# Optimization experiments

Measured on AMD Instinct MI355X. Metric: run time of the kernel, lower is better.

The kernel has to match this reference:

```python
import jax, jax.numpy as jnp
import numpy as np

B, N, DIM = 4, 2048, 768
H, C = 12, 64            # num_heads, head_dim
M = 384                  # num random features = dim * kernel_ratio
SCALE = C ** (-0.25)
EPS = 1e-8
INV_SQRT_M = 1.0 / np.sqrt(M).astype(np.float32)


def _make_orf(key):
    # per-head orthogonal random features: rows of each (C, M) block are
    # orthonormal (C <= M), scaled by sqrt(M), matching sample_orf's intent.
    g = jax.random.normal(key, (H, M, C), jnp.float32)
    q = jnp.linalg.qr(g)[0]                 # (H, M, C), orthonormal columns
    return jnp.transpose(q, (0, 2, 1)) * np.float32(np.sqrt(M))  # (H, C, M)


def setup_inputs() -> dict:
    key = jax.random.key(0)
    k0, k1, k2, k3 = jax.random.split(key, 4)
    x = jax.random.normal(k0, (B, N, DIM), jnp.float32)
    w = _make_orf(k1)                                       # (H, C, M), frozen
    Wqkv = jax.random.normal(k2, (DIM, 3 * DIM), jnp.float32) * 0.02
    Wproj = jax.random.normal(k3, (DIM, DIM), jnp.float32) * 0.02
    bproj = jnp.zeros((DIM,), jnp.float32)
    return {"x": x, "w": w, "Wqkv": Wqkv, "Wproj": Wproj, "bproj": bproj}


def _kernel(x, w):
    # x: (B, H, N, C) -> phi(x): (B, H, N, M)
    xs = x * SCALE
    proj = jnp.einsum('bhnc,hcm->bhnm', xs, w)
    sq_half = 0.5 * jnp.sum(xs * xs, axis=-1, keepdims=True)  # (B,H,N,1)
    return jnp.exp(proj - sq_half) * INV_SQRT_M


def reference(x, w, Wqkv, Wproj, bproj):
    qkv = (x @ Wqkv).reshape(B, N, 3, H, C).transpose(2, 0, 3, 1, 4)
    q, k, v = qkv[0], qkv[1], qkv[2]
    qf = _kernel(q, w)                       # (B, H, N, M)
    kf = _kernel(k, w)                       # (B, H, N, M)
    # normalizer D_n = q'_n . sum_j k'_j
    D = jnp.einsum('bhnm,bhm->bhn', qf, jnp.sum(kf, axis=2)) + EPS
    # linear attention: (k'^T v) then q' @ (k'^T v)
    ktv = jnp.einsum('bhnm,bhnc->bhmc', kf, v)      # (B, H, M, C)
    out = jnp.einsum('bhnm,bhmc->bhnc', qf, ktv) / D[..., None]
    out = out.transpose(0, 2, 1, 3).reshape(B, N, DIM)
    return out @ Wproj + bproj
```

## Files before the change

### kernel.cpp

```cpp
#include <hip/hip_runtime.h>

typedef __attribute__((ext_vector_type(8))) short s16x8;
typedef __attribute__((ext_vector_type(4))) float f32x4;

#define MFMA(a, b, c) __builtin_amdgcn_mfma_f32_16x16x32_bf16(a, b, c, 0, 0, 0)

namespace {

constexpr int Bn = 4, Nn = 2048, Hn = 12, Mn = 384;
constexpr float SCALE = 0.35355339059327379f;
constexpr float ISM = 0.05103103630798288f;
constexpr float EPS = 1e-8f;

__device__ inline unsigned short f2b(float f) {
  unsigned u = __builtin_bit_cast(unsigned, f);
  return (unsigned short)((u + 0x7fffu + ((u >> 16) & 1u)) >> 16);
}
__device__ inline float b2f(unsigned short h) {
  unsigned u = ((unsigned)h) << 16;
  return __builtin_bit_cast(float, u);
}

__device__ inline void gl_lds16(const unsigned short* g, unsigned short* l) {
  __builtin_amdgcn_global_load_lds(
      (const __attribute__((address_space(1))) unsigned int*)g,
      (__attribute__((address_space(3))) unsigned int*)l, 16, 0, 0);
}

__global__ __launch_bounds__(256) void cvt_all_k(const float* __restrict__ x,
                                                 const float* __restrict__ Wqkv,
                                                 const float* __restrict__ Wproj,
                                                 const float* __restrict__ w,
                                                 unsigned short* __restrict__ xb,
                                                 unsigned short* __restrict__ wqT,
                                                 unsigned short* __restrict__ wpT,
                                                 unsigned short* __restrict__ wt) {
  const int bid = blockIdx.x;
  if (bid < 3072) {
    const int id = bid * 256 + threadIdx.x;
    const float* src = x + (size_t)id * 8;
    s16x8 o;
#pragma unroll
    for (int j = 0; j < 8; ++j) o[j] = (short)f2b(src[j]);
    *(s16x8*)(xb + (size_t)id * 8) = o;
  } else if (bid < 3936) {
    const int id = (bid - 3072) * 256 + threadIdx.x;
    const int n = id / 96, kc = (id % 96) * 8;
    s16x8 o;
#pragma unroll
    for (int j = 0; j < 8; ++j) o[j] = (short)f2b(Wqkv[(size_t)(kc + j) * 2304 + n]);
    *(s16x8*)(wqT + (size_t)n * 768 + kc) = o;
  } else if (bid < 4224) {
    const int id = (bid - 3936) * 256 + threadIdx.x;
    const int n = id / 96, kc = (id % 96) * 8;
    s16x8 o;
#pragma unroll
    for (int j = 0; j < 8; ++j) o[j] = (short)f2b(Wproj[(size_t)(kc + j) * 768 + n]);
    *(s16x8*)(wpT + (size_t)n * 768 + kc) = o;
  } else {
    const int id = (bid - 4224) * 256 + threadIdx.x;
    const int h = id / (384 * 8);
    const int r = id % (384 * 8);
    const int m = r / 8, cc = (r % 8) * 8;
    s16x8 o;
#pragma unroll
    for (int j = 0; j < 8; ++j) o[j] = (short)f2b(w[((size_t)h * 64 + cc + j) * 384 + m]);
    *(s16x8*)(wt + ((size_t)h * 384 + m) * 64 + cc) = o;
  }
}

__global__ __launch_bounds__(256) void gemm_qkv_k(const unsigned short* __restrict__ A,
                                                  const unsigned short* __restrict__ Bt,
                                                  unsigned short* __restrict__ obf) {
  __shared__ unsigned short ldsA[128 * 64];
  __shared__ unsigned short ldsB[128 * 64];
  char* lA = (char*)ldsA;
  char* lB = (char*)ldsB;
  const int t = threadIdx.x, lane = t & 63, w = t >> 6;
  const int ln = lane & 15, kg = lane >> 4;
  const int flat = blockIdx.y * 18 + blockIdx.x;
  const int swz = (flat & 7) * 144 + (flat >> 3);
  const size_t bm = (size_t)(swz / 18) * 128, bn = (size_t)(swz % 18) * 128;
  const int wr = w >> 1, wc = w & 1;
  const int sr = lane >> 3, s = lane & 7;
  f32x4 acc[4][4];
#pragma unroll
  for (int i = 0; i < 4; ++i)
#pragma unroll
    for (int j = 0; j < 4; ++j) acc[i][j] = (f32x4){0.f, 0.f, 0.f, 0.f};

  for (int kb = 0; kb < 768; kb += 64) {
    __syncthreads();
#pragma unroll
    for (int c = 0; c < 4; ++c) {
      const int row = c * 32 + w * 8 + sr;
      const int ss = (s ^ (row & 7)) * 8;
      gl_lds16(A + (bm + row) * 768 + kb + ss, ldsA + (c * 4 + w) * 512);
      gl_lds16(Bt + (bn + row) * 768 + kb + ss, ldsB + (c * 4 + w) * 512);
    }
    __syncthreads();
#pragma unroll
    for (int ks = 0; ks < 2; ++ks) {
      s16x8 af[4], bfr[4];
#pragma unroll
      for (int mi = 0; mi < 4; ++mi) {
        const int row = wr * 64 + mi * 16 + ln;
        af[mi] = *(const s16x8*)(lA + row * 128 + (((ks * 4 + kg) ^ (row & 7)) << 4));
      }
#pragma unroll
      for (int ni = 0; ni < 4; ++ni) {
        const int row = wc * 64 + ni * 16 + ln;
        bfr[ni] = *(const s16x8*)(lB + row * 128 + (((ks * 4 + kg) ^ (row & 7)) << 4));
      }
#pragma unroll
      for (int mi = 0; mi < 4; ++mi)
#pragma unroll
        for (int ni = 0; ni < 4; ++ni) acc[mi][ni] = MFMA(af[mi], bfr[ni], acc[mi][ni]);
    }
  }
#pragma unroll
  for (int mi = 0; mi < 4; ++mi)
#pragma unroll
    for (int ni = 0; ni < 4; ++ni) {
      const size_t orow0 = bm + wr * 64 + mi * 16 + kg * 4;
      const size_t ocol = bn + wc * 64 + ni * 16 + ln;
#pragma unroll
      for (int r = 0; r < 4; ++r) obf[(orow0 + r) * 2304 + ocol] = f2b(acc[mi][ni][r]);
    }
}

__global__ __launch_bounds__(256) void gemm_proj_k(const unsigned short* __restrict__ A,
                                                   const unsigned short* __restrict__ Bt,
                                                   float* __restrict__ out,
                                                   const float* __restrict__ bias) {
  __shared__ unsigned short ldsA[128 * 64];
  __shared__ unsigned short ldsB[64 * 64];
  char* lA = (char*)ldsA;
  char* lB = (char*)ldsB;
  const int t = threadIdx.x, lane = t & 63, w = t >> 6;
  const int ln = lane & 15, kg = lane >> 4;
  const int flat = blockIdx.y * 12 + blockIdx.x;
  const int swz = (flat & 7) * 96 + (flat >> 3);
  const size_t bm = (size_t)(swz / 12) * 128, bn = (size_t)(swz % 12) * 64;
  const int wr = w >> 1, wc = w & 1;
  const int sr = lane >> 3, s = lane & 7;
  f32x4 acc[4][2];
#pragma unroll
  for (int i = 0; i < 4; ++i)
#pragma unroll
    for (int j = 0; j < 2; ++j) acc[i][j] = (f32x4){0.f, 0.f, 0.f, 0.f};

  for (int kb = 0; kb < 768; kb += 64) {
    __syncthreads();
#pragma unroll
    for (int c = 0; c < 4; ++c) {
      const int row = c * 32 + w * 8 + sr;
      const int ss = (s ^ (row & 7)) * 8;
      gl_lds16(A + (bm + row) * 768 + kb + ss, ldsA + (c * 4 + w) * 512);
    }
#pragma unroll
    for (int c = 0; c < 2; ++c) {
      const int row = c * 32 + w * 8 + sr;
      const int ss = (s ^ (row & 7)) * 8;
      gl_lds16(Bt + (bn + row) * 768 + kb + ss, ldsB + (c * 4 + w) * 512);
    }
    __syncthreads();
#pragma unroll
    for (int ks = 0; ks < 2; ++ks) {
      s16x8 af[4], bfr[2];
#pragma unroll
      for (int mi = 0; mi < 4; ++mi) {
        const int row = wr * 64 + mi * 16 + ln;
        af[mi] = *(const s16x8*)(lA + row * 128 + (((ks * 4 + kg) ^ (row & 7)) << 4));
      }
#pragma unroll
      for (int ni = 0; ni < 2; ++ni) {
        const int row = wc * 32 + ni * 16 + ln;
        bfr[ni] = *(const s16x8*)(lB + row * 128 + (((ks * 4 + kg) ^ (row & 7)) << 4));
      }
#pragma unroll
      for (int mi = 0; mi < 4; ++mi)
#pragma unroll
        for (int ni = 0; ni < 2; ++ni) acc[mi][ni] = MFMA(af[mi], bfr[ni], acc[mi][ni]);
    }
  }
#pragma unroll
  for (int mi = 0; mi < 4; ++mi)
#pragma unroll
    for (int ni = 0; ni < 2; ++ni) {
      const size_t orow0 = bm + wr * 64 + mi * 16 + kg * 4;
      const size_t ocol = bn + wc * 32 + ni * 16 + ln;
      const float bv = bias[ocol];
#pragma unroll
      for (int r = 0; r < 4; ++r) out[(orow0 + r) * 768 + ocol] = acc[mi][ni][r] + bv;
    }
}

template <int NCT, int CT0>
__device__ inline void s2_gemm2(const char* kfT_b, const char* vt_b, int mts, int ln, int kg,
                                f32x4 (*acc)[3]) {
#pragma unroll
  for (int half = 0; half < 2; ++half) {
    s16x8 a[3], bb[NCT];
#pragma unroll
    for (int j = 0; j < 3; ++j) {
      const int m = (mts + j) * 16 + ln;
      a[j] = *(const s16x8*)(kfT_b + m * 128 + ((half * 64 + kg * 16) ^ ((m & 7) << 4)));
    }
#pragma unroll
    for (int i = 0; i < NCT; ++i) {
      const int c = (CT0 + i) * 16 + ln;
      bb[i] = *(const s16x8*)(vt_b + c * 128 + ((half * 64 + kg * 16) ^ ((c & 7) << 4)));
    }
#pragma unroll
    for (int j = 0; j < 3; ++j)
#pragma unroll
      for (int i = 0; i < NCT; ++i) acc[j][i] = MFMA(a[j], bb[i], acc[j][i]);
  }
}

__global__ __launch_bounds__(512, 4) void stage2_k(const unsigned short* __restrict__ qkv,
                                                   const unsigned short* __restrict__ wt,
                                                   float* __restrict__ ktv_part,
                                                   float* __restrict__ ksum_part) {
  __shared__ unsigned short kfT[192 * 64];
  __shared__ unsigned short vt[80 * 64];
  __shared__ unsigned short wt_s[192 * 64];
  __shared__ unsigned short k_s[64 * 64];
  __shared__ float sqh[64];
  char* kfT_b = (char*)kfT;
  char* vt_b = (char*)vt;
  char* wt_b = (char*)wt_s;
  char* k_b = (char*)k_s;
  const int t = threadIdx.x, lane = t & 63, w = t >> 6;
  const int ln = lane & 15, kg = lane >> 4;
  const int gx = blockIdx.x, h = blockIdx.y, b = blockIdx.z;
  const int ng = gx >> 1, mh = gx & 1, m0 = mh * 192;
  const int bh = b * Hn + h;
  const int ntile = w & 3, mgrp = w >> 2;
  const int mts = (w & 3) * 3;
  const int cg = w >> 2;
  const int lr = lane >> 3, sl = lane & 7;

  auto stage_k = [&](int ch) {
    const int row = w * 8 + lr;
    gl_lds16(qkv + ((size_t)b * Nn + ng * 512 + ch * 64 + row) * 2304 + 768 + h * 64 +
                 ((sl ^ (row & 7)) * 8),
             k_s + w * 512);
  };
  const int vn = t >> 3, vc0 = (t & 7) * 8;
  auto load_v = [&](int ch) {
    return *(const s16x8*)(qkv + ((size_t)b * Nn + ng * 512 + ch * 64 + vn) * 2304 + 1536 +
                           h * 64 + vc0);
  };
  auto scat_v = [&](s16x8 vv) {
#pragma unroll
    for (int j = 0; j < 8; ++j) {
      const int c = vc0 + j;
      *(unsigned short*)(vt_b + c * 128 + ((2 * vn) ^ ((c & 7) << 4))) = (unsigned short)vv[j];
    }
  };
  auto do_sq = [&]() {
    const int n = t >> 3, slq = t & 7;
    const s16x8 kk = *(const s16x8*)(k_b + n * 128 + ((slq ^ (n & 7)) << 4));
    float sacc = 0.f;
#pragma unroll
    for (int j = 0; j < 8; ++j) {
      const float f = b2f((unsigned short)kk[j]);
      sacc = fmaf(f, f, sacc);
    }
    sacc += __shfl_xor(sacc, 1);
    sacc += __shfl_xor(sacc, 2);
    sacc += __shfl_xor(sacc, 4);
    if ((t & 7) == 0) sqh[n] = 0.5f * SCALE * SCALE * sacc;
  };

#pragma unroll
  for (int rr = 0; rr < 3; ++rr) {
    const int j = w * 3 + rr;
    const int row = j * 8 + lr;
    gl_lds16(wt + ((size_t)h * 384 + m0 + row) * 64 + ((sl ^ (row & 7)) * 8), wt_s + j * 512);
  }
  for (int i = t; i < 1024; i += 512) {
    const int c = 64 + (i >> 6), nn = i & 63;
    *(unsigned short*)(vt_b + c * 128 + ((2 * nn) ^ ((c & 7) << 4))) =
        (c == 64) ? (unsigned short)0x3F80 : (unsigned short)0;
  }
  stage_k(0);
  s16x8 vreg = load_v(0);
  __syncthreads();
  scat_v(vreg);
  do_sq();
  __syncthreads();

  f32x4 acc[3][3];
#pragma unroll
  for (int j = 0; j < 3; ++j)
#pragma unroll
    for (int i = 0; i < 3; ++i) acc[j][i] = (f32x4){0.f, 0.f, 0.f, 0.f};

  for (int ch = 0; ch < 8; ++ch) {
    {
      const int arow = ntile * 16 + ln;
      const s16x8 a0 = *(const s16x8*)(k_b + arow * 128 + ((kg ^ (arow & 7)) << 4));
      const s16x8 a1 = *(const s16x8*)(k_b + arow * 128 + (((kg + 4) ^ (arow & 7)) << 4));
      const int nr = ntile * 16 + kg * 4;
      const float s0 = sqh[nr], s1 = sqh[nr + 1], s2 = sqh[nr + 2], s3 = sqh[nr + 3];
#pragma unroll
      for (int i = 0; i < 6; ++i) {
        const int mloc = (mgrp * 6 + i) * 16 + ln;
        const s16x8 b0 = *(const s16x8*)(wt_b + mloc * 128 + ((kg ^ (mloc & 7)) << 4));
        const s16x8 b1 = *(const s16x8*)(wt_b + mloc * 128 + (((kg + 4) ^ (mloc & 7)) << 4));
        f32x4 p = (f32x4){0.f, 0.f, 0.f, 0.f};
        p = MFMA(a0, b0, p);
        p = MFMA(a1, b1, p);
        const float e0 = __expf(fmaf(SCALE, p[0], -s0)) * ISM;
        const float e1 = __expf(fmaf(SCALE, p[1], -s1)) * ISM;
        const float e2 = __expf(fmaf(SCALE, p[2], -s2)) * ISM;
        const float e3 = __expf(fmaf(SCALE, p[3], -s3)) * ISM;
        uint2 pk;
        pk.x = (unsigned)f2b(e0) | ((unsigned)f2b(e1) << 16);
        pk.y = (unsigned)f2b(e2) | ((unsigned)f2b(e3) << 16);
        const int bytn = 32 * ntile + 8 * kg;
        *(uint2*)(kfT_b + mloc * 128 + (bytn ^ ((mloc & 7) << 4))) = pk;
      }
    }
    __syncthreads();
    if (ch < 7) {
      stage_k(ch + 1);
      vreg = load_v(ch + 1);
    }
    if (cg == 0)
      s2_gemm2<3, 0>(kfT_b, vt_b, mts, ln, kg, acc);
    else
      s2_gemm2<2, 3>(kfT_b, vt_b, mts, ln, kg, acc);
    __syncthreads();
    if (ch < 7) {
      scat_v(vreg);
      do_sq();
      __syncthreads();
    }
  }
  float* base = ktv_part + ((size_t)ng * 48 + bh) * (384 * 64);
  const int nct2 = cg ? 2 : 3, ct0c = cg ? 3 : 0;
#pragma unroll
  for (int j = 0; j < 3; ++j)
#pragma unroll
    for (int i = 0; i < 3; ++i) {
      if (i >= nct2) continue;
      const int ct = ct0c + i;
      const int mrow0 = m0 + (mts + j) * 16 + kg * 4;
      if (ct < 4) {
        const int c = ct * 16 + ln;
#pragma unroll
        for (int r = 0; r < 4; ++r) base[(size_t)(mrow0 + r) * 64 + c] = acc[j][i][r];
      } else if (ln == 0) {
#pragma unroll
        for (int r = 0; r < 4; ++r)
          ksum_part[((size_t)ng * 48 + bh) * 384 + mrow0 + r] = acc[j][i][r];
      }
    }
}

__global__ __launch_bounds__(256) void reduce_all_k(const float* __restrict__ part,
                                                    const float* __restrict__ partk,
                                                    unsigned short* __restrict__ ktve) {
  const int bid = blockIdx.x;
  if (bid < 4608) {
    const int bh = bid / 96, chunk = bid % 96;
    const int idx = chunk * 256 + threadIdx.x;
    const int m = idx >> 6, c = idx & 63;
    const size_t o = (size_t)bh * 24576 + idx;
    const size_t gs = (size_t)48 * 24576;
    const float s = part[o] + part[o + gs] + part[o + 2 * gs] + part[o + 3 * gs];
    ktve[((size_t)bh * 80 + c) * 384 + m] = f2b(s);
  } else {
    const int idx = (bid - 4608) * 256 + threadIdx.x;
    const int bh = idx / 384, m = idx % 384;
    const int gs = 48 * 384;
    const float s = partk[idx] + partk[idx + gs] + partk[idx + 2 * gs] + partk[idx + 3 * gs];
    const unsigned short hi = f2b(s);
    const unsigned short lo = f2b(s - b2f(hi));
    const size_t base = ((size_t)bh * 80 + 64) * 384 + m;
    ktve[base] = hi;
    ktve[base + 384] = lo;
  }
}

__global__ __launch_bounds__(512, 4) void stage3_k(const unsigned short* __restrict__ qkv,
                                                   const unsigned short* __restrict__ wt,
                                                   const unsigned short* __restrict__ ktve,
                                                   unsigned short* __restrict__ attn) {
  __shared__ unsigned short q_s[128 * 64];
  __shared__ unsigned short qf_s[128 * 64];
  __shared__ unsigned short wt_s[2][64 * 64];
  __shared__ unsigned short kt_s[2][80 * 64];
  char* q_b = (char*)q_s;
  char* qf_b = (char*)qf_s;
  const int t = threadIdx.x, lane = t & 63, w = t >> 6;
  const int ln = lane & 15, kg = lane >> 4;
  const int nb = blockIdx.x, h = blockIdx.y, b = blockIdx.z, bh = b * Hn + h;
  const size_t tok0 = (size_t)b * Nn + nb * 128;
  const int lr = lane >> 3, sl = lane & 7;

#pragma unroll
  for (int rr = 0; rr < 2; ++rr) {
    const int row = w * 16 + rr * 8 + lr;
    gl_lds16(qkv + (tok0 + row) * 2304 + h * 64 + ((sl ^ (row & 7)) * 8),
             q_s + (w * 16 + rr * 8) * 64 + lane * 8);
  }
  auto stage_wt = [&](int mc, int pb) {
    const int row = w * 8 + lr;
    gl_lds16(wt + ((size_t)h * 384 + mc * 64 + row) * 64 + ((sl ^ (row & 7)) * 8),
             wt_s[pb] + w * 512 + lane * 8);
  };
  auto stage_kt = [&](int mc, int pb) {
    const int row = w * 8 + lr;
    gl_lds16(ktve + ((size_t)bh * 80 + row) * 384 + mc * 64 + ((sl ^ (row & 7)) * 8),
             kt_s[pb] + w * 512 + lane * 8);
    if (w < 2) {
      const int row2 = 64 + w * 8 + lr;
      gl_lds16(ktve + ((size_t)bh * 80 + row2) * 384 + mc * 64 + ((sl ^ (row2 & 7)) * 8),
               kt_s[pb] + (64 + w * 8) * 64 + lane * 8);
    }
  };
  stage_wt(0, 0);
  stage_kt(0, 0);
  __syncthreads();

  f32x4 acc2[5];
#pragma unroll
  for (int i = 0; i < 5; ++i) acc2[i] = (f32x4){0.f, 0.f, 0.f, 0.f};

  const int arow = w * 16 + ln;
  const char* qrow = q_b + arow * 128;
  const int asw = (arow & 7) << 4;

  for (int mc = 0; mc < 6; ++mc) {
    const int pb = mc & 1;
    if (mc < 5) {
      stage_wt(mc + 1, pb ^ 1);
      stage_kt(mc + 1, pb ^ 1);
    }
    const s16x8 af0 = *(const s16x8*)(qrow + ((kg << 4) ^ asw));
    const s16x8 af1 = *(const s16x8*)(qrow + (((kg + 4) << 4) ^ asw));
    const char* wb = (const char*)wt_s[pb];
    f32x4 p[4];
#pragma unroll
    for (int mt = 0; mt < 4; ++mt) {
      const int mrow = mt * 16 + ln;
      const s16x8 b0 = *(const s16x8*)(wb + mrow * 128 + ((kg ^ (mrow & 7)) << 4));
      const s16x8 b1 = *(const s16x8*)(wb + mrow * 128 + (((kg + 4) ^ (mrow & 7)) << 4));
      f32x4 pp = (f32x4){0.f, 0.f, 0.f, 0.f};
      pp = MFMA(af0, b0, pp);
      p[mt] = MFMA(af1, b1, pp);
    }
#pragma unroll
    for (int mt = 0; mt < 4; ++mt) {
#pragma unroll
      for (int r = 0; r < 4; ++r) {
        const int trow = w * 16 + kg * 4 + r;
        const int m = mt * 16 + ln;
        *(unsigned short*)(qf_b + trow * 128 + ((2 * m) ^ ((trow & 7) << 4))) =
            f2b(__expf(SCALE * p[mt][r]));
      }
    }
    const char* qfr = qf_b + arow * 128;
    const s16x8 a0 = *(const s16x8*)(qfr + ((kg << 4) ^ asw));
    const s16x8 a1 = *(const s16x8*)(qfr + (((kg + 4) << 4) ^ asw));
    const char* kb = (const char*)kt_s[pb];
#pragma unroll
    for (int ct = 0; ct < 5; ++ct) {
      const int crow = ct * 16 + ln;
      const s16x8 b0 = *(const s16x8*)(kb + crow * 128 + ((kg ^ (crow & 7)) << 4));
      const s16x8 b1 = *(const s16x8*)(kb + crow * 128 + (((kg + 4) ^ (crow & 7)) << 4));
      acc2[ct] = MFMA(a0, b0, acc2[ct]);
      acc2[ct] = MFMA(a1, b1, acc2[ct]);
    }
    __syncthreads();
  }
  float dv[4];
#pragma unroll
  for (int r = 0; r < 4; ++r) {
    const float hi = __shfl(acc2[4][r], (lane & 48));
    const float lo = __shfl(acc2[4][r], (lane & 48) | 1);
    dv[r] = 1.0f / (hi + lo + EPS);
  }
#pragma unroll
  for (int ct = 0; ct < 4; ++ct) {
#pragma unroll
    for (int r = 0; r < 4; ++r) {
      const int trow = w * 16 + kg * 4 + r;
      const int c = ct * 16 + ln;
      attn[(tok0 + trow) * 768 + h * 64 + c] = f2b(acc2[ct][r] * dv[r]);
    }
  }
}

}

extern "C" void kernel_launch(void* const* d_in, const int* in_sizes, int n_in,
                              void* d_out, int out_size, void* d_ws, size_t ws_size,
                              hipStream_t stream) {
  const float* x = (const float*)d_in[0];
  const float* w = (const float*)d_in[1];
  const float* Wqkv = (const float*)d_in[2];
  const float* Wproj = (const float*)d_in[3];
  const float* bproj = (const float*)d_in[4];

  char* ws = (char*)d_ws;
  unsigned short* xb = (unsigned short*)(ws);
  unsigned short* wqT = (unsigned short*)(ws + 12582912);
  float* ktv_part = (float*)(ws);
  float* ksum_part = (float*)(ws + 18874368);
  char* p = ws + 19169280;
  unsigned short* qkvb = (unsigned short*)p;  p += 37748736;
  unsigned short* wt = (unsigned short*)p;    p += 589824;
  unsigned short* ktve = (unsigned short*)p;  p += 2949120;
  unsigned short* attn = (unsigned short*)p;  p += 12582912;
  unsigned short* wpT = (unsigned short*)p;

  cvt_all_k<<<4368, 256, 0, stream>>>(x, Wqkv, Wproj, w, xb, wqT, wpT, wt);
  gemm_qkv_k<<<dim3(18, 64), 256, 0, stream>>>(xb, wqT, qkvb);
  stage2_k<<<dim3(8, 12, 4), 512, 0, stream>>>(qkvb, wt, ktv_part, ksum_part);
  reduce_all_k<<<4680, 256, 0, stream>>>(ktv_part, ksum_part, ktve);
  stage3_k<<<dim3(16, 12, 4), 512, 0, stream>>>(qkvb, wt, ktve, attn);
  gemm_proj_k<<<dim3(12, 64), 256, 0, stream>>>(attn, wpT, (float*)d_out, bproj);
}
```

Baseline: 149.6 us.

## Double-buffer LDS tiles in QKV and output projection GEMMs

Both projection GEMMs now use two LDS buffers. The next K-tile is prefetched with global_load_lds while the current tile feeds the MFMAs, and partial vmcnt waits plus raw s_barrier replace the two __syncthreads per iteration. The goal is to hide global load latency behind compute. In exchange, LDS use per block doubles, which can lower occupancy, and correctness depends on the hand-written vmcnt counts matching the number of loads issued per stage.

```diff
diff --git a/kernel.cpp b/kernel.cpp
--- a/kernel.cpp
+++ b/kernel.cpp
@@ -72,10 +72,8 @@
 __global__ __launch_bounds__(256) void gemm_qkv_k(const unsigned short* __restrict__ A,
                                                   const unsigned short* __restrict__ Bt,
                                                   unsigned short* __restrict__ obf) {
-  __shared__ unsigned short ldsA[128 * 64];
-  __shared__ unsigned short ldsB[128 * 64];
-  char* lA = (char*)ldsA;
-  char* lB = (char*)ldsB;
+  __shared__ unsigned short ldsA[2][128 * 64];
+  __shared__ unsigned short ldsB[2][128 * 64];
   const int t = threadIdx.x, lane = t & 63, w = t >> 6;
   const int ln = lane & 15, kg = lane >> 4;
   const int flat = blockIdx.y * 18 + blockIdx.x;
@@ -89,16 +87,29 @@
 #pragma unroll
     for (int j = 0; j < 4; ++j) acc[i][j] = (f32x4){0.f, 0.f, 0.f, 0.f};
 
-  for (int kb = 0; kb < 768; kb += 64) {
-    __syncthreads();
+  auto stage = [&](int kb, int d) {
 #pragma unroll
     for (int c = 0; c < 4; ++c) {
       const int row = c * 32 + w * 8 + sr;
       const int ss = (s ^ (row & 7)) * 8;
-      gl_lds16(A + (bm + row) * 768 + kb + ss, ldsA + (c * 4 + w) * 512);
-      gl_lds16(Bt + (bn + row) * 768 + kb + ss, ldsB + (c * 4 + w) * 512);
-    }
-    __syncthreads();
+      gl_lds16(A + (bm + row) * 768 + kb + ss, &ldsA[d][(c * 4 + w) * 512]);
+      gl_lds16(Bt + (bn + row) * 768 + kb + ss, &ldsB[d][(c * 4 + w) * 512]);
+    }
+  };
+
+  stage(0, 0);
+  for (int ti = 0; ti < 12; ++ti) {
+    const int cur = ti & 1;
+    if (ti < 11) {
+      stage((ti + 1) * 64, cur ^ 1);
+      asm volatile("s_waitcnt vmcnt(8)" ::: "memory");
+    } else {
+      asm volatile("s_waitcnt vmcnt(0)" ::: "memory");
+    }
+    __builtin_amdgcn_s_barrier();
+    asm volatile("" ::: "memory");
+    const char* lA = (const char*)ldsA[cur];
+    const char* lB = (const char*)ldsB[cur];
 #pragma unroll
     for (int ks = 0; ks < 2; ++ks) {
       s16x8 af[4], bfr[4];
@@ -117,6 +128,9 @@
 #pragma unroll
         for (int ni = 0; ni < 4; ++ni) acc[mi][ni] = MFMA(af[mi], bfr[ni], acc[mi][ni]);
     }
+    asm volatile("" ::: "memory");
+    __builtin_amdgcn_s_barrier();
+    asm volatile("" ::: "memory");
   }
 #pragma unroll
   for (int mi = 0; mi < 4; ++mi)
@@ -133,10 +147,8 @@
                                                    const unsigned short* __restrict__ Bt,
                                                    float* __restrict__ out,
                                                    const float* __restrict__ bias) {
-  __shared__ unsigned short ldsA[128 * 64];
-  __shared__ unsigned short ldsB[64 * 64];
-  char* lA = (char*)ldsA;
-  char* lB = (char*)ldsB;
+  __shared__ unsigned short ldsA[2][128 * 64];
+  __shared__ unsigned short ldsB[2][64 * 64];
   const int t = threadIdx.x, lane = t & 63, w = t >> 6;
   const int ln = lane & 15, kg = lane >> 4;
   const int flat = blockIdx.y * 12 + blockIdx.x;
@@ -150,21 +162,34 @@
 #pragma unroll
     for (int j = 0; j < 2; ++j) acc[i][j] = (f32x4){0.f, 0.f, 0.f, 0.f};
 
-  for (int kb = 0; kb < 768; kb += 64) {
-    __syncthreads();
+  auto stage = [&](int kb, int d) {
 #pragma unroll
     for (int c = 0; c < 4; ++c) {
       const int row = c * 32 + w * 8 + sr;
       const int ss = (s ^ (row & 7)) * 8;
-      gl_lds16(A + (bm + row) * 768 + kb + ss, ldsA + (c * 4 + w) * 512);
+      gl_lds16(A + (bm + row) * 768 + kb + ss, &ldsA[d][(c * 4 + w) * 512]);
     }
 #pragma unroll
     for (int c = 0; c < 2; ++c) {
       const int row = c * 32 + w * 8 + sr;
       const int ss = (s ^ (row & 7)) * 8;
-      gl_lds16(Bt + (bn + row) * 768 + kb + ss, ldsB + (c * 4 + w) * 512);
-    }
-    __syncthreads();
+      gl_lds16(Bt + (bn + row) * 768 + kb + ss, &ldsB[d][(c * 4 + w) * 512]);
+    }
+  };
+
+  stage(0, 0);
+  for (int ti = 0; ti < 12; ++ti) {
+    const int cur = ti & 1;
+    if (ti < 11) {
+      stage((ti + 1) * 64, cur ^ 1);
+      asm volatile("s_waitcnt vmcnt(6)" ::: "memory");
+    } else {
+      asm volatile("s_waitcnt vmcnt(0)" ::: "memory");
+    }
+    __builtin_amdgcn_s_barrier();
+    asm volatile("" ::: "memory");
+    const char* lA = (const char*)ldsA[cur];
+    const char* lB = (const char*)ldsB[cur];
 #pragma unroll
     for (int ks = 0; ks < 2; ++ks) {
       s16x8 af[4], bfr[2];
@@ -183,6 +208,9 @@
 #pragma unroll
         for (int ni = 0; ni < 2; ++ni) acc[mi][ni] = MFMA(af[mi], bfr[ni], acc[mi][ni]);
     }
+    asm volatile("" ::: "memory");
+    __builtin_amdgcn_s_barrier();
+    asm volatile("" ::: "memory");
   }
 #pragma unroll
   for (int mi = 0; mi < 4; ++mi)
```

New measurement: 150.3 us. No clear change (+0.5%).

## Double-buffer V tile and compute key norms from MFMA fragments

Applied to the files above, without the earlier changes.

The transposed V tile in LDS becomes a two-slot buffer, so the next chunk's V can be scattered while the current chunk's GEMM reads the other slot. This removes one block-wide barrier per chunk iteration. The separate squared-norm pass through shared memory is dropped: each lane now computes the row norm from the K fragments it already holds in registers and combines it with lane shuffles. The trade-off is about 10 KB more LDS per block and some extra shuffle and ALU work per chunk.

```diff
diff --git a/kernel.cpp b/kernel.cpp
--- a/kernel.cpp
+++ b/kernel.cpp
@@ -224,12 +224,10 @@
                                                    float* __restrict__ ktv_part,
                                                    float* __restrict__ ksum_part) {
   __shared__ unsigned short kfT[192 * 64];
-  __shared__ unsigned short vt[80 * 64];
+  __shared__ unsigned short vt[2][80 * 64];
   __shared__ unsigned short wt_s[192 * 64];
   __shared__ unsigned short k_s[64 * 64];
-  __shared__ float sqh[64];
   char* kfT_b = (char*)kfT;
-  char* vt_b = (char*)vt;
   char* wt_b = (char*)wt_s;
   char* k_b = (char*)k_s;
   const int t = threadIdx.x, lane = t & 63, w = t >> 6;
@@ -253,26 +251,13 @@
     return *(const s16x8*)(qkv + ((size_t)b * Nn + ng * 512 + ch * 64 + vn) * 2304 + 1536 +
                            h * 64 + vc0);
   };
-  auto scat_v = [&](s16x8 vv) {
+  auto scat_v = [&](s16x8 vv, int buf) {
+    char* vb = (char*)vt[buf];
 #pragma unroll
     for (int j = 0; j < 8; ++j) {
       const int c = vc0 + j;
-      *(unsigned short*)(vt_b + c * 128 + ((2 * vn) ^ ((c & 7) << 4))) = (unsigned short)vv[j];
-    }
-  };
-  auto do_sq = [&]() {
-    const int n = t >> 3, slq = t & 7;
-    const s16x8 kk = *(const s16x8*)(k_b + n * 128 + ((slq ^ (n & 7)) << 4));
-    float sacc = 0.f;
-#pragma unroll
-    for (int j = 0; j < 8; ++j) {
-      const float f = b2f((unsigned short)kk[j]);
-      sacc = fmaf(f, f, sacc);
-    }
-    sacc += __shfl_xor(sacc, 1);
-    sacc += __shfl_xor(sacc, 2);
-    sacc += __shfl_xor(sacc, 4);
-    if ((t & 7) == 0) sqh[n] = 0.5f * SCALE * SCALE * sacc;
+      *(unsigned short*)(vb + c * 128 + ((2 * vn) ^ ((c & 7) << 4))) = (unsigned short)vv[j];
+    }
   };
 
 #pragma unroll
@@ -281,16 +266,16 @@
     const int row = j * 8 + lr;
     gl_lds16(wt + ((size_t)h * 384 + m0 + row) * 64 + ((sl ^ (row & 7)) * 8), wt_s + j * 512);
   }
-  for (int i = t; i < 1024; i += 512) {
-    const int c = 64 + (i >> 6), nn = i & 63;
-    *(unsigned short*)(vt_b + c * 128 + ((2 * nn) ^ ((c & 7) << 4))) =
+  for (int i = t; i < 2048; i += 512) {
+    const int buf = i >> 10, r = i & 1023;
+    const int c = 64 + (r >> 6), nn = r & 63;
+    *(unsigned short*)((char*)vt[buf] + c * 128 + ((2 * nn) ^ ((c & 7) << 4))) =
         (c == 64) ? (unsigned short)0x3F80 : (unsigned short)0;
   }
   stage_k(0);
   s16x8 vreg = load_v(0);
   __syncthreads();
-  scat_v(vreg);
-  do_sq();
+  scat_v(vreg, 0);
   __syncthreads();
 
   f32x4 acc[3][3];
@@ -298,14 +283,28 @@
   for (int j = 0; j < 3; ++j)
 #pragma unroll
     for (int i = 0; i < 3; ++i) acc[j][i] = (f32x4){0.f, 0.f, 0.f, 0.f};
+
+  const float sqc = 0.5f * SCALE * SCALE;
 
   for (int ch = 0; ch < 8; ++ch) {
     {
       const int arow = ntile * 16 + ln;
       const s16x8 a0 = *(const s16x8*)(k_b + arow * 128 + ((kg ^ (arow & 7)) << 4));
       const s16x8 a1 = *(const s16x8*)(k_b + arow * 128 + (((kg + 4) ^ (arow & 7)) << 4));
-      const int nr = ntile * 16 + kg * 4;
-      const float s0 = sqh[nr], s1 = sqh[nr + 1], s2 = sqh[nr + 2], s3 = sqh[nr + 3];
+      float sq = 0.f;
+#pragma unroll
+      for (int j = 0; j < 8; ++j) {
+        const float f0 = b2f((unsigned short)a0[j]);
+        const float f1 = b2f((unsigned short)a1[j]);
+        sq = fmaf(f0, f0, sq);
+        sq = fmaf(f1, f1, sq);
+      }
+      sq += __shfl_xor(sq, 16);
+      sq += __shfl_xor(sq, 32);
+      const int kg4 = (lane >> 4) << 2;
+      float sqv[4];
+#pragma unroll
+      for (int r = 0; r < 4; ++r) sqv[r] = sqc * __shfl(sq, kg4 + r);
 #pragma unroll
       for (int i = 0; i < 6; ++i) {
         const int mloc = (mgrp * 6 + i) * 16 + ln;
@@ -314,10 +313,10 @@
         f32x4 p = (f32x4){0.f, 0.f, 0.f, 0.f};
         p = MFMA(a0, b0, p);
         p = MFMA(a1, b1, p);
-        const float e0 = __expf(fmaf(SCALE, p[0], -s0)) * ISM;
-        const float e1 = __expf(fmaf(SCALE, p[1], -s1)) * ISM;
-        const float e2 = __expf(fmaf(SCALE, p[2], -s2)) * ISM;
-        const float e3 = __expf(fmaf(SCALE, p[3], -s3)) * ISM;
+        const float e0 = __expf(fmaf(SCALE, p[0], -sqv[0])) * ISM;
+        const float e1 = __expf(fmaf(SCALE, p[1], -sqv[1])) * ISM;
+        const float e2 = __expf(fmaf(SCALE, p[2], -sqv[2])) * ISM;
+        const float e3 = __expf(fmaf(SCALE, p[3], -sqv[3])) * ISM;
         uint2 pk;
         pk.x = (unsigned)f2b(e0) | ((unsigned)f2b(e1) << 16);
         pk.y = (unsigned)f2b(e2) | ((unsigned)f2b(e3) << 16);
@@ -330,16 +329,13 @@
       stage_k(ch + 1);
       vreg = load_v(ch + 1);
     }
+    const char* vt_cur = (const char*)vt[ch & 1];
     if (cg == 0)
-      s2_gemm2<3, 0>(kfT_b, vt_b, mts, ln, kg, acc);
+      s2_gemm2<3, 0>(kfT_b, vt_cur, mts, ln, kg, acc);
     else
-      s2_gemm2<2, 3>(kfT_b, vt_b, mts, ln, kg, acc);
-    __syncthreads();
-    if (ch < 7) {
-      scat_v(vreg);
-      do_sq();
-      __syncthreads();
-    }
+      s2_gemm2<2, 3>(kfT_b, vt_cur, mts, ln, kg, acc);
+    if (ch < 7) scat_v(vreg, (ch + 1) & 1);
+    __syncthreads();
   }
   float* base = ktv_part + ((size_t)ng * 48 + bh) * (384 * 64);
   const int nct2 = cg ? 2 : 3, ct0c = cg ? 3 : 0;
```

New measurement: 149.7 us. Within noise of the previous version (+0.0%).
